# Performance work log

Hardware: AMD Instinct MI355X
Metric: run time of the kernel (lower is better)

## Reference

```python
import jax, jax.numpy as jnp
import numpy as np

HIDDEN = 8

def _offdiag_cols(A: int) -> np.ndarray:
    # cols[i] = all column indices except i, shape (A, A-1)
    idx = np.arange(A)
    return np.stack([np.delete(idx, i) for i in range(A)], axis=0).astype(np.int32)

def setup_inputs() -> dict:
    key = jax.random.key(0)
    k1, k2, k3, k4, k5 = jax.random.split(key, 5)
    T, B, A, N = 512, 32, 64, 128
    H = HIDDEN
    scale = 1.0 / np.sqrt(N)
    return {
        "agent_state": jax.random.normal(k1, (T, B, A, N), dtype=jnp.float32),
        "Wq": jax.random.uniform(k2, (N, H), jnp.float32, -scale, scale),
        "bq": jax.random.uniform(k3, (H,), jnp.float32, -scale, scale),
        "Wk": jax.random.uniform(k4, (N, H), jnp.float32, -scale, scale),
        "bk": jax.random.uniform(k5, (H,), jnp.float32, -scale, scale),
    }

def reference(agent_state, Wq, bq, Wk, bk):
    T, B, A, N = agent_state.shape
    H = Wq.shape[1]
    query = agent_state @ Wq + bq                      # (T,B,A,H)
    key_ = agent_state @ Wk + bk                       # (T,B,A,H)
    # faithful to original: reshape (NOT transpose) to (T,B,H,A)
    key_ = key_.reshape(T, B, H, A)
    att = jnp.matmul(query, key_)                      # (T,B,A,A)
    att = jax.nn.softmax(att / jnp.sqrt(jnp.float32(1.0)), axis=-1)
    # remove diagonal: gather off-diagonal columns per row -> (T,B,A,A-1)
    cols = jnp.asarray(_offdiag_cols(A))               # (A, A-1)
    return jnp.take_along_axis(att, cols[None, None, :, :], axis=-1)
```

## Files before the change

kernel.cpp:

```cpp
#include <hip/hip_runtime.h>
#include <cstdint>
#include <cstddef>

#define A_DIM 64
#define N_DIM 128
#define H_DIM 8
#define OUT_PER_BLK (A_DIM * (A_DIM - 1))
#define ATT_STRIDE 68

__global__ __launch_bounds__(256, 4) void attn_kernel(
    const float* __restrict__ S,
    const float* __restrict__ Wq,
    const float* __restrict__ bq,
    const float* __restrict__ Wk,
    const float* __restrict__ bk,
    float* __restrict__ out)
{
    __shared__ float smem[A_DIM * ATT_STRIDE];
    __shared__ float q_lds[A_DIM * H_DIM];
    __shared__ float k_lds[A_DIM * H_DIM];

    const int tid  = threadIdx.x;
    const int blk  = blockIdx.x;
    const int lane = tid & 63;
    const int wv   = __builtin_amdgcn_readfirstlane(tid >> 6);

    const int n0 = wv * 32;
    const float* srow = S + (size_t)blk * (A_DIM * N_DIM) + (size_t)lane * N_DIM + n0;
    float sb[32];
    {
        const float4* sp = (const float4*)srow;
        #pragma unroll
        for (int c = 0; c < 8; ++c) {
            float4 v = sp[c];
            sb[4*c+0] = v.x; sb[4*c+1] = v.y; sb[4*c+2] = v.z; sb[4*c+3] = v.w;
        }
    }

    float qa[H_DIM] = {0,0,0,0,0,0,0,0};
    float ka[H_DIM] = {0,0,0,0,0,0,0,0};
    #pragma unroll
    for (int j = 0; j < 32; ++j) {
        const float s = sb[j];
        const float* wqj = Wq + (n0 + j) * H_DIM;
        const float* wkj = Wk + (n0 + j) * H_DIM;
        #pragma unroll
        for (int h = 0; h < H_DIM; ++h) {
            qa[h] = fmaf(s, wqj[h], qa[h]);
            ka[h] = fmaf(s, wkj[h], ka[h]);
        }
    }
    {
        float* p = smem + wv * (16 * 64) + lane;
        #pragma unroll
        for (int h = 0; h < H_DIM; ++h) {
            p[h * 64]       = qa[h];
            p[(8 + h) * 64] = ka[h];
        }
    }
    __syncthreads();

    {
        const int ii = tid >> 2;
        const int h2 = tid & 3;
        float v0 = 0.f, v1 = 0.f, v2 = 0.f, v3 = 0.f;
        #pragma unroll
        for (int w = 0; w < 4; ++w) {
            const float* p = smem + w * (16 * 64) + ii;
            v0 += p[(h2     ) * 64];
            v1 += p[(h2 +  4) * 64];
            v2 += p[(h2 +  8) * 64];
            v3 += p[(h2 + 12) * 64];
        }
        q_lds[ii * 8 + h2    ] = v0 + bq[h2];
        q_lds[ii * 8 + h2 + 4] = v1 + bq[h2 + 4];
        k_lds[ii * 8 + h2    ] = v2 + bk[h2];
        k_lds[ii * 8 + h2 + 4] = v3 + bk[h2 + 4];
    }
    __syncthreads();

    const int i  = tid >> 2;
    const int jb = tid & 3;
    float qv[H_DIM];
    #pragma unroll
    for (int h = 0; h < H_DIM; ++h) qv[h] = q_lds[i * 8 + h];

    float acc[16];
    #pragma unroll
    for (int c = 0; c < 16; ++c) acc[c] = 0.f;
    #pragma unroll
    for (int h = 0; h < H_DIM; ++h) {
        const float* kr = k_lds + h * 64 + jb * 16;
        const float qh = qv[h];
        #pragma unroll
        for (int c = 0; c < 16; ++c) acc[c] = fmaf(qh, kr[c], acc[c]);
    }

    float m = acc[0];
    #pragma unroll
    for (int c = 1; c < 16; ++c) m = fmaxf(m, acc[c]);
    m = fmaxf(m, __shfl_xor(m, 1, 64));
    m = fmaxf(m, __shfl_xor(m, 2, 64));
    float ssum = 0.f;
    #pragma unroll
    for (int c = 0; c < 16; ++c) { acc[c] = __expf(acc[c] - m); ssum += acc[c]; }
    ssum += __shfl_xor(ssum, 1, 64);
    ssum += __shfl_xor(ssum, 2, 64);
    const float inv = 1.0f / ssum;

    {
        float* ar = smem + i * ATT_STRIDE + jb * 16;
        #pragma unroll
        for (int c = 0; c < 16; ++c) ar[c] = acc[c] * inv;
    }
    __syncthreads();

    float4* out4 = (float4*)(out + (size_t)blk * OUT_PER_BLK);
    #pragma unroll
    for (int it = 0; it < 4; ++it) {
        const int o4 = it * 256 + tid;
        if (o4 < OUT_PER_BLK / 4) {
            float tmp[4];
            #pragma unroll
            for (int e = 0; e < 4; ++e) {
                const int idx = o4 * 4 + e;
                const int ii  = idx / 63;
                const int kk  = idx - ii * 63;
                const int jj  = kk + (kk >= ii ? 1 : 0);
                tmp[e] = smem[ii * ATT_STRIDE + jj];
            }
            out4[o4] = make_float4(tmp[0], tmp[1], tmp[2], tmp[3]);
        }
    }
}

extern "C" void kernel_launch(void* const* d_in, const int* in_sizes, int n_in,
                              void* d_out, int out_size, void* d_ws, size_t ws_size,
                              hipStream_t stream) {
    const float* S  = (const float*)d_in[0];
    const float* Wq = (const float*)d_in[1];
    const float* bq = (const float*)d_in[2];
    const float* Wk = (const float*)d_in[3];
    const float* bk = (const float*)d_in[4];
    float* out = (float*)d_out;

    const int n_blocks = in_sizes[0] / (A_DIM * N_DIM);
    attn_kernel<<<dim3(n_blocks), dim3(256), 0, stream>>>(S, Wq, bq, Wk, bk, out);
}
```

Baseline: 761.4 us.

## Process eight tiles per block with double-buffered register prefetch of inputs

Makes each block persistent over eight (T,B) tiles and double-buffers the input rows in registers, so the global load for the next tile is issued before the current tile is computed. The plain __syncthreads calls become an explicit lgkmcnt wait plus s_barrier, and a trailing barrier lets the shared memory be reused across tiles. The occupancy hint drops from 4 to 3 blocks per SM to make room for the extra registers. The grid is now 8x smaller and assumes the tile count divides by 8, which lowers parallelism and adds register pressure.

```diff
diff --git a/kernel.cpp b/kernel.cpp
--- a/kernel.cpp
+++ b/kernel.cpp
@@ -7,41 +7,32 @@
 #define H_DIM 8
 #define OUT_PER_BLK (A_DIM * (A_DIM - 1))
 #define ATT_STRIDE 68
+#define TILES_PER_BLK 8
 
-__global__ __launch_bounds__(256, 4) void attn_kernel(
-    const float* __restrict__ S,
-    const float* __restrict__ Wq,
-    const float* __restrict__ bq,
-    const float* __restrict__ Wk,
-    const float* __restrict__ bk,
-    float* __restrict__ out)
+__device__ __forceinline__ void sync_lds() {
+    asm volatile("s_waitcnt lgkmcnt(0)" ::: "memory");
+    __builtin_amdgcn_s_barrier();
+    __builtin_amdgcn_sched_barrier(0);
+}
+
+#define SB_ELEM(b, j) (((j) & 3) == 0 ? (b)[(j) >> 2].x : \
+                       ((j) & 3) == 1 ? (b)[(j) >> 2].y : \
+                       ((j) & 3) == 2 ? (b)[(j) >> 2].z : (b)[(j) >> 2].w)
+
+__device__ __forceinline__ void compute_tile(
+    const float4 (&sb4)[8], int blk,
+    int tid, int lane, int wv,
+    const float* __restrict__ Wq, const float* __restrict__ bq,
+    const float* __restrict__ Wk, const float* __restrict__ bk,
+    float* __restrict__ out,
+    float* smem, float* q_lds, float* k_lds)
 {
-    __shared__ float smem[A_DIM * ATT_STRIDE];
-    __shared__ float q_lds[A_DIM * H_DIM];
-    __shared__ float k_lds[A_DIM * H_DIM];
-
-    const int tid  = threadIdx.x;
-    const int blk  = blockIdx.x;
-    const int lane = tid & 63;
-    const int wv   = __builtin_amdgcn_readfirstlane(tid >> 6);
-
     const int n0 = wv * 32;
-    const float* srow = S + (size_t)blk * (A_DIM * N_DIM) + (size_t)lane * N_DIM + n0;
-    float sb[32];
-    {
-        const float4* sp = (const float4*)srow;
-        #pragma unroll
-        for (int c = 0; c < 8; ++c) {
-            float4 v = sp[c];
-            sb[4*c+0] = v.x; sb[4*c+1] = v.y; sb[4*c+2] = v.z; sb[4*c+3] = v.w;
-        }
-    }
-
     float qa[H_DIM] = {0,0,0,0,0,0,0,0};
     float ka[H_DIM] = {0,0,0,0,0,0,0,0};
     #pragma unroll
     for (int j = 0; j < 32; ++j) {
-        const float s = sb[j];
+        const float s = SB_ELEM(sb4, j);
         const float* wqj = Wq + (n0 + j) * H_DIM;
         const float* wkj = Wk + (n0 + j) * H_DIM;
         #pragma unroll
@@ -58,7 +49,7 @@
             p[(8 + h) * 64] = ka[h];
         }
     }
-    __syncthreads();
+    sync_lds();
 
     {
         const int ii = tid >> 2;
@@ -77,7 +68,7 @@
         k_lds[ii * 8 + h2    ] = v2 + bk[h2];
         k_lds[ii * 8 + h2 + 4] = v3 + bk[h2 + 4];
     }
-    __syncthreads();
+    sync_lds();
 
     const int i  = tid >> 2;
     const int jb = tid & 3;
@@ -113,7 +104,7 @@
         #pragma unroll
         for (int c = 0; c < 16; ++c) ar[c] = acc[c] * inv;
     }
-    __syncthreads();
+    sync_lds();
 
     float4* out4 = (float4*)(out + (size_t)blk * OUT_PER_BLK);
     #pragma unroll
@@ -132,6 +123,53 @@
             out4[o4] = make_float4(tmp[0], tmp[1], tmp[2], tmp[3]);
         }
     }
+    sync_lds();
+}
+
+__global__ __launch_bounds__(256, 3) void attn_kernel(
+    const float* __restrict__ S,
+    const float* __restrict__ Wq,
+    const float* __restrict__ bq,
+    const float* __restrict__ Wk,
+    const float* __restrict__ bk,
+    float* __restrict__ out)
+{
+    __shared__ float smem[A_DIM * ATT_STRIDE];
+    __shared__ float q_lds[A_DIM * H_DIM];
+    __shared__ float k_lds[A_DIM * H_DIM];
+
+    const int tid  = threadIdx.x;
+    const int lane = tid & 63;
+    const int wv   = __builtin_amdgcn_readfirstlane(tid >> 6);
+    const int blk0 = blockIdx.x * TILES_PER_BLK;
+
+    const float* sbase = S + (size_t)blk0 * (A_DIM * N_DIM)
+                           + (size_t)lane * N_DIM + (size_t)(wv * 32);
+
+    float4 sbA[8], sbB[8];
+
+    {
+        const float4* sp = (const float4*)sbase;
+        #pragma unroll
+        for (int c = 0; c < 8; ++c) sbA[c] = sp[c];
+    }
+
+    #pragma unroll 1
+    for (int t = 0; t < TILES_PER_BLK; t += 2) {
+        {
+            const float4* sp = (const float4*)(sbase + (size_t)(t + 1) * (A_DIM * N_DIM));
+            #pragma unroll
+            for (int c = 0; c < 8; ++c) sbB[c] = sp[c];
+        }
+        compute_tile(sbA, blk0 + t, tid, lane, wv, Wq, bq, Wk, bk, out, smem, q_lds, k_lds);
+
+        if (t + 2 < TILES_PER_BLK) {
+            const float4* sp = (const float4*)(sbase + (size_t)(t + 2) * (A_DIM * N_DIM));
+            #pragma unroll
+            for (int c = 0; c < 8; ++c) sbA[c] = sp[c];
+        }
+        compute_tile(sbB, blk0 + t + 1, tid, lane, wv, Wq, bq, Wk, bk, out, smem, q_lds, k_lds);
+    }
 }
 
 extern "C" void kernel_launch(void* const* d_in, const int* in_sizes, int n_in,
@@ -144,6 +182,7 @@
     const float* bk = (const float*)d_in[4];
     float* out = (float*)d_out;
 
-    const int n_blocks = in_sizes[0] / (A_DIM * N_DIM);
+    const int n_tiles  = in_sizes[0] / (A_DIM * N_DIM);
+    const int n_blocks = n_tiles / TILES_PER_BLK;
     attn_kernel<<<dim3(n_blocks), dim3(256), 0, stream>>>(S, Wq, bq, Wk, bk, out);
 }
```

New measurement: 803.3 us. +5.5%, slower.
